# Optimization experiments

Hardware: AMD Instinct MI355X
Metric: run time of the kernel (lower is better)

Reference implementation:

```python
import jax, jax.numpy as jnp
import numpy as np

B, NQ, NK = 2, 1024, 8192
DIM, CTX_DIM = 512, 512
HEADS, DIM_HEAD = 8, 64
INNER = HEADS * DIM_HEAD
EPS = 1e-5
SCALE = DIM_HEAD ** -0.5


def layernorm(x, w, b):
    m = jnp.mean(x, axis=-1, keepdims=True)
    v = jnp.var(x, axis=-1, keepdims=True)
    return (x - m) * jax.lax.rsqrt(v + EPS) * w + b


def rotate_half(x):
    # interleaved pairs: (..., 2i, 2i+1) -> (-x[2i+1], x[2i])
    x1 = x[..., 0::2]
    x2 = x[..., 1::2]
    return jnp.stack((-x2, x1), axis=-1).reshape(x.shape)


def apply_rope(freqs, x):
    # freqs: (b, n, d) broadcast over heads; x: (b, h, n, d)
    f = freqs[:, None, :, :]
    return x * jnp.cos(f) + rotate_half(x) * jnp.sin(f)


def setup_inputs() -> dict:
    key = jax.random.key(0)
    ks = jax.random.split(key, 12)
    x_query = jax.random.normal(ks[0], (B, NQ, DIM), jnp.float32)
    x_context = jax.random.normal(ks[1], (B, NK, CTX_DIM), jnp.float32)
    rotary_q = jax.random.uniform(ks[2], (B, NQ, DIM_HEAD), jnp.float32) * 6.28
    rotary_c = jax.random.uniform(ks[3], (B, NK, DIM_HEAD), jnp.float32) * 6.28
    attn_mask = jax.random.uniform(ks[4], (B, NK)) > 0.1
    attn_mask = attn_mask.at[:, 0].set(True)  # ensure >=1 valid key per row
    s_q = (1.0 / DIM) ** 0.5
    s_c = (1.0 / CTX_DIM) ** 0.5
    s_o = (1.0 / INNER) ** 0.5
    return {
        'x_query': x_query,
        'x_context': x_context,
        'rotary_q': rotary_q,
        'rotary_c': rotary_c,
        'attn_mask': attn_mask,
        'norm_w': jnp.ones((DIM,), jnp.float32),
        'norm_b': jnp.zeros((DIM,), jnp.float32),
        'norm_ctx_w': jnp.ones((CTX_DIM,), jnp.float32),
        'norm_ctx_b': jnp.zeros((CTX_DIM,), jnp.float32),
        'w_q': jax.random.uniform(ks[5], (DIM, INNER), jnp.float32, -s_q, s_q),
        'w_kv': jax.random.uniform(ks[6], (CTX_DIM, 2 * INNER), jnp.float32, -s_c, s_c),
        'w_out': jax.random.uniform(ks[7], (INNER, DIM), jnp.float32, -s_o, s_o),
        'b_out': jax.random.uniform(ks[8], (DIM,), jnp.float32, -s_o, s_o),
    }


def reference(x_query, x_context, rotary_q, rotary_c, attn_mask,
              norm_w, norm_b, norm_ctx_w, norm_ctx_b, w_q, w_kv, w_out, b_out):
    xq = layernorm(x_query, norm_w, norm_b)
    xc = layernorm(x_context, norm_ctx_w, norm_ctx_b)
    q = jnp.einsum('bnd,de->bne', xq, w_q)
    kv = jnp.einsum('bnd,de->bne', xc, w_kv)
    k, v = jnp.split(kv, 2, axis=-1)
    split_heads = lambda t: t.reshape(t.shape[0], t.shape[1], HEADS, DIM_HEAD).transpose(0, 2, 1, 3)
    q, k, v = split_heads(q), split_heads(k), split_heads(v)
    q = apply_rope(rotary_q, q)
    k = apply_rope(rotary_c, k)
    v = apply_rope(rotary_c, v)  # rotate_value=True
    scores = jnp.einsum('bhqd,bhkd->bhqk', q, k) * SCALE
    scores = jnp.where(attn_mask[:, None, None, :], scores, jnp.finfo(scores.dtype).min)
    attn = jax.nn.softmax(scores, axis=-1)
    out = jnp.einsum('bhqk,bhkd->bhqd', attn, v)
    out = apply_rope(-rotary_q, out)  # inverse rotation of output
    out = out.transpose(0, 2, 1, 3).reshape(out.shape[0], NQ, INNER)
    return jnp.einsum('bne,ed->bnd', out, w_out) + b_out
```

## Files before the change

kernel.cpp:

```cpp
#include <hip/hip_runtime.h>
#include <math.h>

typedef __attribute__((ext_vector_type(8))) short  short8;
typedef __attribute__((ext_vector_type(4))) float  f32x4;
typedef __attribute__((ext_vector_type(4))) unsigned short u16x4;
typedef __attribute__((ext_vector_type(8))) unsigned short u16x8;
typedef unsigned short u16;

#define B_     2
#define NQ_    1024
#define NK_    8192
#define DIM_   512
#define H_     8
#define DH_    64
#define EPS_   1e-5f
#define SCALE_ 0.125f
#define LOG2E_ 1.4426950408889634f

__device__ __forceinline__ u16 f2bf(float f) {
  unsigned int u = __float_as_uint(f);
  u += 0x7fffu + ((u >> 16) & 1u);
  return (u16)(u >> 16);
}
__device__ __forceinline__ float fmax3(float a, float b, float c) {
  return fmaxf(fmaxf(a, b), c);
}

__global__ __launch_bounds__(256) void prep_kernel(
    const float* __restrict__ wq, const float* __restrict__ wkv,
    const float* __restrict__ wout,
    const float* __restrict__ xq, const float* __restrict__ xc,
    const float* __restrict__ nw, const float* __restrict__ nb,
    const float* __restrict__ ncw, const float* __restrict__ ncb,
    const float* __restrict__ rq, const float* __restrict__ rc,
    const int* __restrict__ mask,
    u16* __restrict__ wqT, u16* __restrict__ wkvT, u16* __restrict__ woutT,
    u16* __restrict__ xqb, u16* __restrict__ xcb,
    float* __restrict__ cq, float* __restrict__ sq2,
    float* __restrict__ cc, float* __restrict__ sc2,
    float* __restrict__ maskf) {
  __shared__ float tile[64][65];
  const int bid = blockIdx.x;
  const int t = threadIdx.x;
  if (bid < 256) {
    const float* W; u16* WT; int N; int tix;
    if (bid < 64)       { W = wq;   WT = wqT;   N = 512;  tix = bid; }
    else if (bid < 192) { W = wkv;  WT = wkvT;  N = 1024; tix = bid - 64; }
    else                { W = wout; WT = woutT; N = 512;  tix = bid - 192; }
    int ntn = N >> 6;
    int k0 = (tix / ntn) << 6, n0 = (tix % ntn) << 6;
    {
      int kk = t >> 2, nc = (t & 3) << 4;
#pragma unroll
      for (int i = 0; i < 4; ++i) {
        f32x4 v = *(const f32x4*)&W[(size_t)(k0 + kk) * N + n0 + nc + 4 * i];
        tile[kk][nc + 4*i + 0] = v[0];
        tile[kk][nc + 4*i + 1] = v[1];
        tile[kk][nc + 4*i + 2] = v[2];
        tile[kk][nc + 4*i + 3] = v[3];
      }
    }
    __syncthreads();
    {
      int n = t >> 2, kc = (t & 3) << 4;
#pragma unroll
      for (int i = 0; i < 2; ++i) {
        u16x8 o;
#pragma unroll
        for (int j = 0; j < 8; ++j) o[j] = f2bf(tile[kc + 8*i + j][n]);
        *(u16x8*)&WT[(size_t)(n0 + n) * 512 + k0 + kc + 8*i] = o;
      }
    }
  } else if (bid < 4864) {
    int wid = t >> 6, lane = t & 63;
    int row = (bid - 256) * 4 + wid;
    const float* x; const float* w; const float* bb; u16* o; int r;
    if (row < 2048) { x = xq; w = nw;  bb = nb;  o = xqb; r = row; }
    else            { x = xc; w = ncw; bb = ncb; o = xcb; r = row - 2048; }
    const f32x4* px = (const f32x4*)(x + (size_t)r * 512);
    f32x4 v0 = px[lane], v1 = px[lane + 64];
    float s  = v0[0]+v0[1]+v0[2]+v0[3] + v1[0]+v1[1]+v1[2]+v1[3];
    float ss = v0[0]*v0[0]+v0[1]*v0[1]+v0[2]*v0[2]+v0[3]*v0[3]
             + v1[0]*v1[0]+v1[1]*v1[1]+v1[2]*v1[2]+v1[3]*v1[3];
#pragma unroll
    for (int ofs = 32; ofs >= 1; ofs >>= 1) { s += __shfl_xor(s, ofs); ss += __shfl_xor(ss, ofs); }
    float mu = s * (1.f/512.f);
    float var = ss * (1.f/512.f) - mu*mu;
    float rs = rsqrtf(var + EPS_);
    const f32x4* pw = (const f32x4*)w; const f32x4* pb = (const f32x4*)bb;
#pragma unroll
    for (int seg = 0; seg < 2; ++seg) {
      int e4 = lane + 64*seg;
      f32x4 xv = seg ? v1 : v0;
      f32x4 wv = pw[e4], bv = pb[e4];
      u16x4 ov;
#pragma unroll
      for (int c = 0; c < 4; ++c) ov[c] = f2bf((xv[c]-mu)*rs*wv[c] + bv[c]);
      *(u16x4*)&o[(size_t)r*512 + e4*4] = ov;
    }
  } else if (bid < 8960) {
    int i = (bid - 4864) * 256 + t;
    const int NQE = B_*NQ_*DH_;
    const int NCE = B_*NK_*DH_;
    if (i < NQE) { float s, c; sincosf(rq[i], &s, &c); cq[i] = c; sq2[i] = s; }
    if (i < NCE) { float s, c; sincosf(rc[i], &s, &c); cc[i] = c; sc2[i] = s; }
  } else {
    int i = (bid - 8960) * 256 + t;
    maskf[i] = mask[i] ? 1.f : 0.f;
  }
}

template<int MODE>
__global__ __launch_bounds__(256) void gemm_mfma(
    const u16* __restrict__ Abf, const u16* __restrict__ WT,
    const float* __restrict__ ctab, const float* __restrict__ stab,
    const float* __restrict__ bias, const float* __restrict__ mvf,
    u16* __restrict__ out0, u16* __restrict__ out1, float* __restrict__ outf) {
  constexpr int BM   = (MODE==1) ? 128 : 64;
  constexpr int BN   = (MODE==1) ? 128 : 32;
  constexpr int MR   = BM/64;
  constexpr int NR   = BN/16;
  constexpr int N    = (MODE==1) ? 1024 : 512;
  constexpr int NSEQ = (MODE==1) ? 8192 : 1024;
  constexpr int NBN  = N / BN;
  constexpr int NWG  = (((MODE==1)?16384:2048)/BM) * NBN;
  __shared__ u16 As[BM*64];
  __shared__ u16 Bs[BN*64];
  const int tid = threadIdx.x;
  const int w = tid >> 6, l = tid & 63;
  const int la = l >> 4, lb = l & 15;
  int bid = blockIdx.x;
  bid = (bid & 7) * (NWG/8) + (bid >> 3);
  const int m0 = (bid / NBN) * BM;
  const int n0 = (bid % NBN) * BN;
  f32x4 acc[MR][NR];
#pragma unroll
  for (int i = 0; i < MR; ++i)
#pragma unroll
    for (int j = 0; j < NR; ++j) acc[i][j] = (f32x4){0.f,0.f,0.f,0.f};

  constexpr int APT = BM/32;
  constexpr int BPT = BN/32;
  const int arow = tid / (8/APT);
  const int ag0  = (tid % (8/APT)) * APT;
  const int brow = tid / (8/BPT);
  const int bg0  = (tid % (8/BPT)) * BPT;

  auto loadA = [&](int k0, int g) -> short8 {
    if (MODE == 2) {
      int kk = k0 + g*8;
      int m = m0 + arow;
      return *(const short8*)&Abf[((size_t)((m >> 10)*H_ + (kk >> 6)) * NQ_ + (m & 1023)) * 64 + (kk & 63)];
    } else {
      return *(const short8*)&Abf[(size_t)(m0 + arow) * 512 + k0 + g*8];
    }
  };

  short8 apre[APT], bpre[BPT];
#pragma unroll
  for (int i = 0; i < APT; ++i) apre[i] = loadA(0, ag0 + i);
#pragma unroll
  for (int i = 0; i < BPT; ++i) bpre[i] = *(const short8*)&WT[(size_t)(n0 + brow) * 512 + (bg0 + i)*8];

  for (int k0 = 0; k0 < 512; k0 += 64) {
    if (k0) __syncthreads();
#pragma unroll
    for (int i = 0; i < APT; ++i) {
      int g = ag0 + i;
      *(short8*)&As[arow*64 + ((g ^ (arow & 7)) << 3)] = apre[i];
    }
#pragma unroll
    for (int i = 0; i < BPT; ++i) {
      int g = bg0 + i;
      *(short8*)&Bs[brow*64 + ((g ^ (brow & 7)) << 3)] = bpre[i];
    }
    if (k0 + 64 < 512) {
#pragma unroll
      for (int i = 0; i < APT; ++i) apre[i] = loadA(k0 + 64, ag0 + i);
#pragma unroll
      for (int i = 0; i < BPT; ++i) bpre[i] = *(const short8*)&WT[(size_t)(n0 + brow) * 512 + (k0+64) + (bg0 + i)*8];
    }
    __syncthreads();
#pragma unroll
    for (int h = 0; h < 2; ++h) {
      short8 af[MR], bfr[NR];
#pragma unroll
      for (int i = 0; i < MR; ++i) {
        int row = w*(16*MR) + i*16 + lb;
        int g = (4*h + la) ^ (row & 7);
        af[i] = *(const short8*)&As[row*64 + g*8];
      }
#pragma unroll
      for (int j = 0; j < NR; ++j) {
        int row = j*16 + lb;
        int g = (4*h + la) ^ (row & 7);
        bfr[j] = *(const short8*)&Bs[row*64 + g*8];
      }
#pragma unroll
      for (int i = 0; i < MR; ++i)
#pragma unroll
        for (int j = 0; j < NR; ++j)
          acc[i][j] = __builtin_amdgcn_mfma_f32_16x16x32_bf16(af[i], bfr[j], acc[i][j], 0, 0, 0);
    }
  }

  if (MODE == 2) {
#pragma unroll
    for (int i = 0; i < MR; ++i)
#pragma unroll
      for (int j = 0; j < NR; ++j) {
        int n = n0 + 16*j + lb;
        float bv = bias[n];
#pragma unroll
        for (int r = 0; r < 4; ++r) {
          int m = m0 + w*(16*MR) + 16*i + 4*la + r;
          outf[(size_t)m * 512 + n] = acc[i][j][r] + bv;
        }
      }
  } else if (MODE == 1 && n0 >= 512) {
#pragma unroll
    for (int i = 0; i < MR; ++i) {
      int mbase = m0 + w*(16*MR) + 16*i + 4*la;
      int bI = mbase >> 13;
      int seq = mbase & 8191;
      f32x4 mkv = *(const f32x4*)&mvf[mbase];
#pragma unroll
      for (int j = 0; j < NR; ++j) {
        int n = n0 + 16*j + lb;
        int e = n - 512, hh = e >> 6, dh = e & 63;
        u16x4 pk4;
#pragma unroll
        for (int r = 0; r < 4; ++r) {
          int m = mbase + r;
          float x = acc[i][j][r];
          float pr = __shfl_xor(x, 1);
          float cv = ctab[(size_t)m*64 + dh];
          float sv = stab[(size_t)m*64 + dh];
          pk4[r] = f2bf((x*cv + ((n & 1) ? pr*sv : -pr*sv)) * mkv[r]);
        }
        *(u16x4*)&out1[((size_t)(bI*H_ + hh)*64 + dh)*8192 + seq] = pk4;
      }
    }
  } else {
#pragma unroll
    for (int i = 0; i < MR; ++i)
#pragma unroll
      for (int j = 0; j < NR; ++j) {
        int n = n0 + 16*j + lb;
        int hh = n >> 6, dh = n & 63;
#pragma unroll
        for (int r = 0; r < 4; ++r) {
          int m = m0 + w*(16*MR) + 16*i + 4*la + r;
          float x = acc[i][j][r];
          float pr = __shfl_xor(x, 1);
          float cv = ctab[(size_t)m*64 + dh];
          float sv = stab[(size_t)m*64 + dh];
          float y = x*cv + ((n & 1) ? pr*sv : -pr*sv);
          if (MODE == 0) y *= SCALE_ * LOG2E_;
          int bI = m / NSEQ, seq = m % NSEQ;
          out0[((size_t)(bI*H_ + hh) * NSEQ + seq) * 64 + dh] = f2bf(y);
        }
      }
  }
}

template<int NS>
__global__ __launch_bounds__(512) void attn_mfma(
    const u16* __restrict__ qb, const u16* __restrict__ kb,
    const u16* __restrict__ vtg, const float* __restrict__ maskf,
    float* __restrict__ Opart, float* __restrict__ mpart, float* __restrict__ lpart) {
  __shared__ u16 Ks[64*64];
  __shared__ u16 Vt[64*64];
  __shared__ u16 Ps[8*16*64];
  constexpr int NWG = 16*8*NS;
  constexpr int CH  = NWG/8;
  constexpr int LS  = (NS==8) ? 3 : 2;
  int orig = blockIdx.x;
  int wid = (orig & 7) * CH + (orig >> 3);
  const int qt = wid & 7;
  const int s  = (wid >> 3) & (NS-1);
  const int bh = wid >> (3 + LS);
  const int bI = bh >> 3;
  const int tid = threadIdx.x;
  const int w = tid >> 6, l = tid & 63;
  const int la = l >> 4, lb = l & 15;
  const int key0 = s * (NK_/NS);

  const int qrow = qt*128 + w*16 + lb;
  short8 qf0 = *(const short8*)&qb[(((size_t)bh * NQ_) + qrow) * 64 + 8*la];
  short8 qf1 = *(const short8*)&qb[(((size_t)bh * NQ_) + qrow) * 64 + 32 + 8*la];

  const int krow = tid >> 3;
  const int kg   = tid & 7;
  const u16* kptr = kb  + ((size_t)bh * NK_ + key0 + krow) * 64;
  const u16* vptr = vtg + ((size_t)bh * 64 + krow) * 8192 + key0;
  short8 kpre = *(const short8*)&kptr[kg*8];
  short8 vpre = *(const short8*)&vptr[kg*8];
  const int ksw = krow & 7;
  const float* mrow = maskf + bI*8192 + key0 + 4*la;

  f32x4 accO[4];
#pragma unroll
  for (int j = 0; j < 4; ++j) accO[j] = (f32x4){0.f,0.f,0.f,0.f};
  float m_run = -1e30f, l_run = 0.f;
  constexpr int NT = (NK_/NS)/64;

  const int pbase = (w*16 + lb)*64;
  const int pwofs = (4*la) & 7;

  for (int kt = 0; kt < NT; ++kt) {
    *(short8*)&Ks[krow*64 + ((kg ^ ksw) << 3)] = kpre;
    *(short8*)&Vt[krow*64 + ((kg ^ ksw) << 3)] = vpre;
    if (kt + 1 < NT) {
      kpre = *(const short8*)&kptr[(kt+1)*4096 + kg*8];
      vpre = *(const short8*)&vptr[(kt+1)*64 + kg*8];
    }
    __syncthreads();

    f32x4 sc[4];
#pragma unroll
    for (int t = 0; t < 4; ++t) sc[t] = (f32x4){0.f,0.f,0.f,0.f};
    __builtin_amdgcn_s_setprio(1);
#pragma unroll
    for (int t = 0; t < 4; ++t) {
      int row = t*16 + lb;
      int g0 = la ^ (row & 7);
      int g1 = (4 + la) ^ (row & 7);
      short8 kf0 = *(const short8*)&Ks[row*64 + g0*8];
      short8 kf1 = *(const short8*)&Ks[row*64 + g1*8];
      sc[t] = __builtin_amdgcn_mfma_f32_16x16x32_bf16(kf0, qf0, sc[t], 0, 0, 0);
      sc[t] = __builtin_amdgcn_mfma_f32_16x16x32_bf16(kf1, qf1, sc[t], 0, 0, 0);
    }
    __builtin_amdgcn_s_setprio(0);
    float a0 = fmax3(sc[0][0], sc[0][1], sc[0][2]);
    float a1 = fmax3(sc[0][3], sc[1][0], sc[1][1]);
    float a2 = fmax3(sc[1][2], sc[1][3], sc[2][0]);
    float a3 = fmax3(sc[2][1], sc[2][2], sc[2][3]);
    float a4 = fmax3(sc[3][0], sc[3][1], sc[3][2]);
    float pmax = fmaxf(fmax3(a0, a1, a2), fmax3(a3, a4, sc[3][3]));
    pmax = fmaxf(pmax, __shfl_xor(pmax, 16));
    pmax = fmaxf(pmax, __shfl_xor(pmax, 32));
    if (!__all(pmax <= m_run + 11.f)) {
      float mnew = fmaxf(m_run, pmax);
      float scl = __builtin_amdgcn_exp2f(m_run - mnew);
      m_run = mnew;
      l_run *= scl;
      float sr[4];
#pragma unroll
      for (int r = 0; r < 4; ++r) sr[r] = __shfl(scl, (l & 48) | (4*la + r));
#pragma unroll
      for (int j = 0; j < 4; ++j)
#pragma unroll
        for (int r = 0; r < 4; ++r) accO[j][r] *= sr[r];
    }
    float l_add = 0.f;
#pragma unroll
    for (int t = 0; t < 4; ++t) {
      f32x4 mk = *(const f32x4*)&mrow[kt*64 + t*16];
      float p0 = __builtin_amdgcn_exp2f(sc[t][0] - m_run);
      float p1 = __builtin_amdgcn_exp2f(sc[t][1] - m_run);
      float p2 = __builtin_amdgcn_exp2f(sc[t][2] - m_run);
      float p3 = __builtin_amdgcn_exp2f(sc[t][3] - m_run);
      l_add = fmaf(p0, mk[0], l_add);
      l_add = fmaf(p1, mk[1], l_add);
      l_add = fmaf(p2, mk[2], l_add);
      l_add = fmaf(p3, mk[3], l_add);
      int gst = 2*t + (la >> 1);
      uint2 pp;
      asm("v_cvt_pk_bf16_f32 %0, %1, %2" : "=v"(pp.x) : "v"(p0), "v"(p1));
      asm("v_cvt_pk_bf16_f32 %0, %1, %2" : "=v"(pp.y) : "v"(p2), "v"(p3));
      *(uint2*)&Ps[pbase + ((gst ^ (lb & 7)) << 3) + pwofs] = pp;
    }
    l_run += l_add;
    __builtin_amdgcn_s_setprio(1);
#pragma unroll
    for (int kh = 0; kh < 2; ++kh) {
      int pg = (4*kh + la) ^ (lb & 7);
      short8 pf = *(const short8*)&Ps[pbase + pg*8];
#pragma unroll
      for (int j = 0; j < 4; ++j) {
        int d = j*16 + lb;
        int vg = (4*kh + la) ^ (d & 7);
        short8 vf = *(const short8*)&Vt[d*64 + vg*8];
        accO[j] = __builtin_amdgcn_mfma_f32_16x16x32_bf16(pf, vf, accO[j], 0, 0, 0);
      }
    }
    __builtin_amdgcn_s_setprio(0);
    __syncthreads();
  }

  l_run += __shfl_xor(l_run, 16);
  l_run += __shfl_xor(l_run, 32);

  const int qa = qt*128 + w*16;
  const size_t obase = ((size_t)s*16 + bh) * 1024;
#pragma unroll
  for (int j = 0; j < 4; ++j)
#pragma unroll
    for (int r = 0; r < 4; ++r)
      Opart[(obase + qa + 4*la + r) * 64 + j*16 + lb] = accO[j][r];
  if (la == 0) {
    mpart[obase + qa + lb] = m_run;
    lpart[obase + qa + lb] = l_run;
  }
}

template<int NS>
__global__ __launch_bounds__(256) void combine_kernel(
    const float* __restrict__ Opart, const float* __restrict__ mpart,
    const float* __restrict__ lpart,
    const float* __restrict__ cosq, const float* __restrict__ sinq,
    u16* __restrict__ aob) {
  const int bid = blockIdx.x;
  const int bh = bid >> 4, qt = bid & 15;
  const int t = threadIdx.x;
  const int ql = t >> 2, ds = (t & 3) << 4;
  const int q = qt*64 + ql;
  const int bI = bh >> 3;
  const size_t rbase = ((size_t)bh << 10) + q;
  float m[NS], li[NS];
  float M = -1e30f;
#pragma unroll
  for (int s = 0; s < NS; ++s) {
    m[s]  = mpart[(size_t)s*16384 + rbase];
    li[s] = lpart[(size_t)s*16384 + rbase];
    M = fmaxf(M, m[s]);
  }
  float ws[NS]; float den = 0.f;
#pragma unroll
  for (int s = 0; s < NS; ++s) { ws[s] = __builtin_amdgcn_exp2f(m[s] - M); den += ws[s]*li[s]; }
  float inv = 1.f / den;
  u16 ob[16];
#pragma unroll
  for (int c = 0; c < 4; ++c) {
    int d0 = ds + 4*c;
    f32x4 o = (f32x4){0.f,0.f,0.f,0.f};
#pragma unroll
    for (int s = 0; s < NS; ++s) {
      f32x4 v = *(const f32x4*)&Opart[((size_t)s*16384 + rbase)*64 + d0];
      o += ws[s] * v;
    }
    o *= inv;
    size_t tix = ((((size_t)bI << 10) + q) << 6) + d0;
    f32x4 cv = *(const f32x4*)&cosq[tix];
    f32x4 sv = *(const f32x4*)&sinq[tix];
    ob[4*c+0] = f2bf(o[0]*cv[0] + o[1]*sv[0]);
    ob[4*c+1] = f2bf(o[1]*cv[1] - o[0]*sv[1]);
    ob[4*c+2] = f2bf(o[2]*cv[2] + o[3]*sv[2]);
    ob[4*c+3] = f2bf(o[3]*cv[3] - o[2]*sv[3]);
  }
  u16x8 w0, w1;
#pragma unroll
  for (int j = 0; j < 8; ++j) { w0[j] = ob[j]; w1[j] = ob[8+j]; }
  *(u16x8*)&aob[rbase*64 + ds]     = w0;
  *(u16x8*)&aob[rbase*64 + ds + 8] = w1;
}

extern "C" void kernel_launch(void* const* d_in, const int* in_sizes, int n_in,
                              void* d_out, int out_size, void* d_ws, size_t ws_size,
                              hipStream_t stream) {
  (void)in_sizes; (void)n_in; (void)out_size;
  const float* xq   = (const float*)d_in[0];
  const float* xc   = (const float*)d_in[1];
  const float* rq   = (const float*)d_in[2];
  const float* rc   = (const float*)d_in[3];
  const int*   mask = (const int*)d_in[4];
  const float* nw   = (const float*)d_in[5];
  const float* nb   = (const float*)d_in[6];
  const float* ncw  = (const float*)d_in[7];
  const float* ncb  = (const float*)d_in[8];
  const float* wq   = (const float*)d_in[9];
  const float* wkv  = (const float*)d_in[10];
  const float* wout = (const float*)d_in[11];
  const float* bout = (const float*)d_in[12];
  float* out = (float*)d_out;

  char* p = (char*)d_ws;
  u16*   woutT  = (u16*)p;   p += 524288;
  float* cosq   = (float*)p; p += 524288;
  float* sinq   = (float*)p; p += 524288;
  u16*   qb     = (u16*)p;   p += 2097152;
  u16*   kb     = (u16*)p;   p += 16777216;
  u16*   vtg    = (u16*)p;   p += 16777216;
  float* mpart4 = (float*)p; p += 262144;
  float* lpart4 = (float*)p; p += 262144;
  u16*   aob    = (u16*)p;   p += 2097152;
  float* maskf  = (float*)aob;
  char* pool = p;
  u16*   wqT   = (u16*)p;   p += 524288;
  u16*   wkvT  = (u16*)p;   p += 1048576;
  u16*   xqb   = (u16*)p;   p += 2097152;
  u16*   xcb   = (u16*)p;   p += 16777216;
  float* cosc  = (float*)p; p += 4194304;
  float* sinc  = (float*)p; p += 4194304;
  float* Opart = (float*)pool;
  float* mpart8 = (float*)(pool + 33554432);
  float* lpart8 = (float*)(pool + 33554432 + 524288);
  const size_t need8 = (size_t)(pool - (char*)d_ws) + 33554432ull + 1048576ull;
  const bool use8 = ws_size >= need8;

  prep_kernel<<<dim3(9024), dim3(256), 0, stream>>>(
      wq, wkv, wout, xq, xc, nw, nb, ncw, ncb, rq, rc, mask,
      wqT, wkvT, woutT, xqb, xcb, cosq, sinq, cosc, sinc, maskf);
  gemm_mfma<0><<<dim3(512), dim3(256), 0, stream>>>(
      xqb, wqT, cosq, sinq, nullptr, nullptr, qb, nullptr, nullptr);
  gemm_mfma<1><<<dim3(1024), dim3(256), 0, stream>>>(
      xcb, wkvT, cosc, sinc, nullptr, maskf, kb, vtg, nullptr);
  if (use8) {
    attn_mfma<8><<<dim3(1024), dim3(512), 0, stream>>>(
        qb, kb, vtg, maskf, Opart, mpart8, lpart8);
    combine_kernel<8><<<dim3(256), dim3(256), 0, stream>>>(
        Opart, mpart8, lpart8, cosq, sinq, aob);
  } else {
    attn_mfma<4><<<dim3(512), dim3(512), 0, stream>>>(
        qb, kb, vtg, maskf, Opart, mpart4, lpart4);
    combine_kernel<4><<<dim3(256), dim3(256), 0, stream>>>(
        Opart, mpart4, lpart4, cosq, sinq, aob);
  }
  gemm_mfma<2><<<dim3(512), dim3(256), 0, stream>>>(
      aob, woutT, nullptr, nullptr, bout, nullptr, nullptr, nullptr, out);
}
```

Before: 209.2 us.

## Merge Q and KV projection launches and retile attention to 64 queries × 128 keys

The Q and KV projection GEMMs now share a single launch, with a device-function body and shared memory passed in, which removes one kernel launch and lets the two run concurrently. The attention kernel moves from 512-thread blocks over 128 queries and 64-key tiles to 256-thread blocks over 64 queries and 128-key tiles, processed as two 64-key chunks per barrier. Split-K is fixed at 4 splits, so the 8-split path that depended on workspace size is gone. This halves the number of barriers and global-load rounds per key, at the cost of fewer waves per block and more shared memory per block.

```diff
diff --git a/kernel.cpp b/kernel.cpp
--- a/kernel.cpp
+++ b/kernel.cpp
@@ -111,7 +111,8 @@
 }
 
 template<int MODE>
-__global__ __launch_bounds__(256) void gemm_mfma(
+__device__ __forceinline__ void gemm_body(
+    int bid0, u16* __restrict__ smem,
     const u16* __restrict__ Abf, const u16* __restrict__ WT,
     const float* __restrict__ ctab, const float* __restrict__ stab,
     const float* __restrict__ bias, const float* __restrict__ mvf,
@@ -124,13 +125,12 @@
   constexpr int NSEQ = (MODE==1) ? 8192 : 1024;
   constexpr int NBN  = N / BN;
   constexpr int NWG  = (((MODE==1)?16384:2048)/BM) * NBN;
-  __shared__ u16 As[BM*64];
-  __shared__ u16 Bs[BN*64];
+  u16* As = smem;
+  u16* Bs = smem + BM*64;
   const int tid = threadIdx.x;
   const int w = tid >> 6, l = tid & 63;
   const int la = l >> 4, lb = l & 15;
-  int bid = blockIdx.x;
-  bid = (bid & 7) * (NWG/8) + (bid >> 3);
+  int bid = (bid0 & 7) * (NWG/8) + (bid0 >> 3);
   const int m0 = (bid / NBN) * BM;
   const int n0 = (bid % NBN) * BN;
   f32x4 acc[MR][NR];
@@ -264,135 +264,178 @@
   }
 }
 
+__global__ __launch_bounds__(256) void qkv_kernel(
+    const u16* __restrict__ xqb, const u16* __restrict__ wqT,
+    const u16* __restrict__ xcb, const u16* __restrict__ wkvT,
+    const float* __restrict__ cosq, const float* __restrict__ sinq,
+    const float* __restrict__ cosc, const float* __restrict__ sinc,
+    const float* __restrict__ maskf,
+    u16* __restrict__ qb, u16* __restrict__ kb, u16* __restrict__ vtg) {
+  __shared__ u16 smem[16384];
+  int b = blockIdx.x;
+  if (b < 512) {
+    gemm_body<0>(b, smem, xqb, wqT, cosq, sinq, nullptr, nullptr, qb, nullptr, nullptr);
+  } else {
+    gemm_body<1>(b - 512, smem, xcb, wkvT, cosc, sinc, nullptr, maskf, kb, vtg, nullptr);
+  }
+}
+
+__global__ __launch_bounds__(256) void gemm2_kernel(
+    const u16* __restrict__ aob, const u16* __restrict__ woutT,
+    const float* __restrict__ bias, float* __restrict__ out) {
+  __shared__ u16 smem[6144];
+  gemm_body<2>(blockIdx.x, smem, aob, woutT, nullptr, nullptr, bias, nullptr,
+               nullptr, nullptr, out);
+}
+
 template<int NS>
-__global__ __launch_bounds__(512) void attn_mfma(
+__global__ __launch_bounds__(256) void attn_mfma(
     const u16* __restrict__ qb, const u16* __restrict__ kb,
     const u16* __restrict__ vtg, const float* __restrict__ maskf,
     float* __restrict__ Opart, float* __restrict__ mpart, float* __restrict__ lpart) {
-  __shared__ u16 Ks[64*64];
-  __shared__ u16 Vt[64*64];
-  __shared__ u16 Ps[8*16*64];
-  constexpr int NWG = 16*8*NS;
+  __shared__ u16 Ks[128*64];
+  __shared__ u16 Vt[64*128];
+  __shared__ u16 Ps[4*16*64];
+  constexpr int NWG = 16*16*NS;
   constexpr int CH  = NWG/8;
   constexpr int LS  = (NS==8) ? 3 : 2;
   int orig = blockIdx.x;
   int wid = (orig & 7) * CH + (orig >> 3);
-  const int qt = wid & 7;
-  const int s  = (wid >> 3) & (NS-1);
-  const int bh = wid >> (3 + LS);
+  const int qt = wid & 15;
+  const int s  = (wid >> 4) & (NS-1);
+  const int bh = wid >> (4 + LS);
   const int bI = bh >> 3;
   const int tid = threadIdx.x;
   const int w = tid >> 6, l = tid & 63;
   const int la = l >> 4, lb = l & 15;
   const int key0 = s * (NK_/NS);
 
-  const int qrow = qt*128 + w*16 + lb;
+  const int qrow = qt*64 + w*16 + lb;
   short8 qf0 = *(const short8*)&qb[(((size_t)bh * NQ_) + qrow) * 64 + 8*la];
   short8 qf1 = *(const short8*)&qb[(((size_t)bh * NQ_) + qrow) * 64 + 32 + 8*la];
 
-  const int krow = tid >> 3;
-  const int kg   = tid & 7;
+  const int krow = tid >> 1;
+  const int kg0  = (tid & 1) * 4;
+  const int vd   = tid >> 2;
+  const int vg0  = (tid & 3) * 4;
   const u16* kptr = kb  + ((size_t)bh * NK_ + key0 + krow) * 64;
-  const u16* vptr = vtg + ((size_t)bh * 64 + krow) * 8192 + key0;
-  short8 kpre = *(const short8*)&kptr[kg*8];
-  short8 vpre = *(const short8*)&vptr[kg*8];
-  const int ksw = krow & 7;
+  const u16* vptr = vtg + ((size_t)bh * 64 + vd) * 8192 + key0;
+  const int ksw = krow & 7, vsw = vd & 7;
+  short8 kpre0 = *(const short8*)&kptr[(kg0+0)*8];
+  short8 kpre1 = *(const short8*)&kptr[(kg0+1)*8];
+  short8 vpre0 = *(const short8*)&vptr[(vg0+0)*8];
+  short8 vpre1 = *(const short8*)&vptr[(vg0+1)*8];
   const float* mrow = maskf + bI*8192 + key0 + 4*la;
 
   f32x4 accO[4];
 #pragma unroll
   for (int j = 0; j < 4; ++j) accO[j] = (f32x4){0.f,0.f,0.f,0.f};
   float m_run = -1e30f, l_run = 0.f;
-  constexpr int NT = (NK_/NS)/64;
+  constexpr int NT = (NK_/NS)/128;
 
   const int pbase = (w*16 + lb)*64;
   const int pwofs = (4*la) & 7;
 
   for (int kt = 0; kt < NT; ++kt) {
-    *(short8*)&Ks[krow*64 + ((kg ^ ksw) << 3)] = kpre;
-    *(short8*)&Vt[krow*64 + ((kg ^ ksw) << 3)] = vpre;
+    short8 k2 = *(const short8*)&kptr[(size_t)kt*8192 + (kg0+2)*8];
+    short8 k3 = *(const short8*)&kptr[(size_t)kt*8192 + (kg0+3)*8];
+    short8 v2 = *(const short8*)&vptr[kt*128 + (vg0+2)*8];
+    short8 v3 = *(const short8*)&vptr[kt*128 + (vg0+3)*8];
+    *(short8*)&Ks[krow*64 + (((kg0+0) ^ ksw) << 3)] = kpre0;
+    *(short8*)&Ks[krow*64 + (((kg0+1) ^ ksw) << 3)] = kpre1;
+    *(short8*)&Vt[vd*128 + (((vg0+0) ^ vsw) << 3)] = vpre0;
+    *(short8*)&Vt[vd*128 + (((vg0+1) ^ vsw) << 3)] = vpre1;
+    *(short8*)&Ks[krow*64 + (((kg0+2) ^ ksw) << 3)] = k2;
+    *(short8*)&Ks[krow*64 + (((kg0+3) ^ ksw) << 3)] = k3;
+    *(short8*)&Vt[vd*128 + (((vg0+2) ^ vsw) << 3)] = v2;
+    *(short8*)&Vt[vd*128 + (((vg0+3) ^ vsw) << 3)] = v3;
     if (kt + 1 < NT) {
-      kpre = *(const short8*)&kptr[(kt+1)*4096 + kg*8];
-      vpre = *(const short8*)&vptr[(kt+1)*64 + kg*8];
+      kpre0 = *(const short8*)&kptr[(size_t)(kt+1)*8192 + (kg0+0)*8];
+      kpre1 = *(const short8*)&kptr[(size_t)(kt+1)*8192 + (kg0+1)*8];
+      vpre0 = *(const short8*)&vptr[(kt+1)*128 + (vg0+0)*8];
+      vpre1 = *(const short8*)&vptr[(kt+1)*128 + (vg0+1)*8];
     }
     __syncthreads();
 
-    f32x4 sc[4];
-#pragma unroll
-    for (int t = 0; t < 4; ++t) sc[t] = (f32x4){0.f,0.f,0.f,0.f};
-    __builtin_amdgcn_s_setprio(1);
-#pragma unroll
-    for (int t = 0; t < 4; ++t) {
-      int row = t*16 + lb;
-      int g0 = la ^ (row & 7);
-      int g1 = (4 + la) ^ (row & 7);
-      short8 kf0 = *(const short8*)&Ks[row*64 + g0*8];
-      short8 kf1 = *(const short8*)&Ks[row*64 + g1*8];
-      sc[t] = __builtin_amdgcn_mfma_f32_16x16x32_bf16(kf0, qf0, sc[t], 0, 0, 0);
-      sc[t] = __builtin_amdgcn_mfma_f32_16x16x32_bf16(kf1, qf1, sc[t], 0, 0, 0);
-    }
-    __builtin_amdgcn_s_setprio(0);
-    float a0 = fmax3(sc[0][0], sc[0][1], sc[0][2]);
-    float a1 = fmax3(sc[0][3], sc[1][0], sc[1][1]);
-    float a2 = fmax3(sc[1][2], sc[1][3], sc[2][0]);
-    float a3 = fmax3(sc[2][1], sc[2][2], sc[2][3]);
-    float a4 = fmax3(sc[3][0], sc[3][1], sc[3][2]);
-    float pmax = fmaxf(fmax3(a0, a1, a2), fmax3(a3, a4, sc[3][3]));
-    pmax = fmaxf(pmax, __shfl_xor(pmax, 16));
-    pmax = fmaxf(pmax, __shfl_xor(pmax, 32));
-    if (!__all(pmax <= m_run + 11.f)) {
-      float mnew = fmaxf(m_run, pmax);
-      float scl = __builtin_amdgcn_exp2f(m_run - mnew);
-      m_run = mnew;
-      l_run *= scl;
-      float sr[4];
-#pragma unroll
-      for (int r = 0; r < 4; ++r) sr[r] = __shfl(scl, (l & 48) | (4*la + r));
-#pragma unroll
-      for (int j = 0; j < 4; ++j)
-#pragma unroll
-        for (int r = 0; r < 4; ++r) accO[j][r] *= sr[r];
-    }
-    float l_add = 0.f;
-#pragma unroll
-    for (int t = 0; t < 4; ++t) {
-      f32x4 mk = *(const f32x4*)&mrow[kt*64 + t*16];
-      float p0 = __builtin_amdgcn_exp2f(sc[t][0] - m_run);
-      float p1 = __builtin_amdgcn_exp2f(sc[t][1] - m_run);
-      float p2 = __builtin_amdgcn_exp2f(sc[t][2] - m_run);
-      float p3 = __builtin_amdgcn_exp2f(sc[t][3] - m_run);
-      l_add = fmaf(p0, mk[0], l_add);
-      l_add = fmaf(p1, mk[1], l_add);
-      l_add = fmaf(p2, mk[2], l_add);
-      l_add = fmaf(p3, mk[3], l_add);
-      int gst = 2*t + (la >> 1);
-      uint2 pp;
-      asm("v_cvt_pk_bf16_f32 %0, %1, %2" : "=v"(pp.x) : "v"(p0), "v"(p1));
-      asm("v_cvt_pk_bf16_f32 %0, %1, %2" : "=v"(pp.y) : "v"(p2), "v"(p3));
-      *(uint2*)&Ps[pbase + ((gst ^ (lb & 7)) << 3) + pwofs] = pp;
-    }
-    l_run += l_add;
-    __builtin_amdgcn_s_setprio(1);
-#pragma unroll
-    for (int kh = 0; kh < 2; ++kh) {
-      int pg = (4*kh + la) ^ (lb & 7);
-      short8 pf = *(const short8*)&Ps[pbase + pg*8];
-#pragma unroll
-      for (int j = 0; j < 4; ++j) {
-        int d = j*16 + lb;
-        int vg = (4*kh + la) ^ (d & 7);
-        short8 vf = *(const short8*)&Vt[d*64 + vg*8];
-        accO[j] = __builtin_amdgcn_mfma_f32_16x16x32_bf16(pf, vf, accO[j], 0, 0, 0);
-      }
-    }
-    __builtin_amdgcn_s_setprio(0);
+#pragma unroll
+    for (int c = 0; c < 2; ++c) {
+      f32x4 sc[4];
+#pragma unroll
+      for (int t = 0; t < 4; ++t) sc[t] = (f32x4){0.f,0.f,0.f,0.f};
+      __builtin_amdgcn_s_setprio(1);
+#pragma unroll
+      for (int t = 0; t < 4; ++t) {
+        int row = c*64 + t*16 + lb;
+        int g0 = la ^ (row & 7);
+        int g1 = (4 + la) ^ (row & 7);
+        short8 kf0 = *(const short8*)&Ks[row*64 + g0*8];
+        short8 kf1 = *(const short8*)&Ks[row*64 + g1*8];
+        sc[t] = __builtin_amdgcn_mfma_f32_16x16x32_bf16(kf0, qf0, sc[t], 0, 0, 0);
+        sc[t] = __builtin_amdgcn_mfma_f32_16x16x32_bf16(kf1, qf1, sc[t], 0, 0, 0);
+      }
+      __builtin_amdgcn_s_setprio(0);
+      float a0 = fmax3(sc[0][0], sc[0][1], sc[0][2]);
+      float a1 = fmax3(sc[0][3], sc[1][0], sc[1][1]);
+      float a2 = fmax3(sc[1][2], sc[1][3], sc[2][0]);
+      float a3 = fmax3(sc[2][1], sc[2][2], sc[2][3]);
+      float a4 = fmax3(sc[3][0], sc[3][1], sc[3][2]);
+      float pmax = fmaxf(fmax3(a0, a1, a2), fmax3(a3, a4, sc[3][3]));
+      pmax = fmaxf(pmax, __shfl_xor(pmax, 16));
+      pmax = fmaxf(pmax, __shfl_xor(pmax, 32));
+      if (!__all(pmax <= m_run + 11.f)) {
+        float mnew = fmaxf(m_run, pmax);
+        float scl = __builtin_amdgcn_exp2f(m_run - mnew);
+        m_run = mnew;
+        l_run *= scl;
+        float sr[4];
+#pragma unroll
+        for (int r = 0; r < 4; ++r) sr[r] = __shfl(scl, (l & 48) | (4*la + r));
+#pragma unroll
+        for (int j = 0; j < 4; ++j)
+#pragma unroll
+          for (int r = 0; r < 4; ++r) accO[j][r] *= sr[r];
+      }
+      float l_add = 0.f;
+#pragma unroll
+      for (int t = 0; t < 4; ++t) {
+        f32x4 mk = *(const f32x4*)&mrow[kt*128 + c*64 + t*16];
+        float p0 = __builtin_amdgcn_exp2f(sc[t][0] - m_run);
+        float p1 = __builtin_amdgcn_exp2f(sc[t][1] - m_run);
+        float p2 = __builtin_amdgcn_exp2f(sc[t][2] - m_run);
+        float p3 = __builtin_amdgcn_exp2f(sc[t][3] - m_run);
+        l_add = fmaf(p0, mk[0], l_add);
+        l_add = fmaf(p1, mk[1], l_add);
+        l_add = fmaf(p2, mk[2], l_add);
+        l_add = fmaf(p3, mk[3], l_add);
+        int gst = 2*t + (la >> 1);
+        uint2 pp;
+        asm("v_cvt_pk_bf16_f32 %0, %1, %2" : "=v"(pp.x) : "v"(p0), "v"(p1));
+        asm("v_cvt_pk_bf16_f32 %0, %1, %2" : "=v"(pp.y) : "v"(p2), "v"(p3));
+        *(uint2*)&Ps[pbase + ((gst ^ (lb & 7)) << 3) + pwofs] = pp;
+      }
+      l_run += l_add;
+      __builtin_amdgcn_s_setprio(1);
+#pragma unroll
+      for (int kh = 0; kh < 2; ++kh) {
+        int pg = (4*kh + la) ^ (lb & 7);
+        short8 pf = *(const short8*)&Ps[pbase + pg*8];
+#pragma unroll
+        for (int j = 0; j < 4; ++j) {
+          int d = j*16 + lb;
+          int vg = (c*8 + 4*kh + la) ^ (d & 7);
+          short8 vf = *(const short8*)&Vt[d*128 + vg*8];
+          accO[j] = __builtin_amdgcn_mfma_f32_16x16x32_bf16(pf, vf, accO[j], 0, 0, 0);
+        }
+      }
+      __builtin_amdgcn_s_setprio(0);
+    }
     __syncthreads();
   }
 
   l_run += __shfl_xor(l_run, 16);
   l_run += __shfl_xor(l_run, 32);
 
-  const int qa = qt*128 + w*16;
+  const int qa = qt*64 + w*16;
   const size_t obase = ((size_t)s*16 + bh) * 1024;
 #pragma unroll
   for (int j = 0; j < 4; ++j)
@@ -459,7 +502,7 @@
 extern "C" void kernel_launch(void* const* d_in, const int* in_sizes, int n_in,
                               void* d_out, int out_size, void* d_ws, size_t ws_size,
                               hipStream_t stream) {
-  (void)in_sizes; (void)n_in; (void)out_size;
+  (void)in_sizes; (void)n_in; (void)out_size; (void)ws_size;
   const float* xq   = (const float*)d_in[0];
   const float* xc   = (const float*)d_in[1];
   const float* rq   = (const float*)d_in[2];
@@ -494,29 +537,15 @@
   float* cosc  = (float*)p; p += 4194304;
   float* sinc  = (float*)p; p += 4194304;
   float* Opart = (float*)pool;
-  float* mpart8 = (float*)(pool + 33554432);
-  float* lpart8 = (float*)(pool + 33554432 + 524288);
-  const size_t need8 = (size_t)(pool - (char*)d_ws) + 33554432ull + 1048576ull;
-  const bool use8 = ws_size >= need8;
 
   prep_kernel<<<dim3(9024), dim3(256), 0, stream>>>(
       wq, wkv, wout, xq, xc, nw, nb, ncw, ncb, rq, rc, mask,
       wqT, wkvT, woutT, xqb, xcb, cosq, sinq, cosc, sinc, maskf);
-  gemm_mfma<0><<<dim3(512), dim3(256), 0, stream>>>(
-      xqb, wqT, cosq, sinq, nullptr, nullptr, qb, nullptr, nullptr);
-  gemm_mfma<1><<<dim3(1024), dim3(256), 0, stream>>>(
-      xcb, wkvT, cosc, sinc, nullptr, maskf, kb, vtg, nullptr);
-  if (use8) {
-    attn_mfma<8><<<dim3(1024), dim3(512), 0, stream>>>(
-        qb, kb, vtg, maskf, Opart, mpart8, lpart8);
-    combine_kernel<8><<<dim3(256), dim3(256), 0, stream>>>(
-        Opart, mpart8, lpart8, cosq, sinq, aob);
-  } else {
-    attn_mfma<4><<<dim3(512), dim3(512), 0, stream>>>(
-        qb, kb, vtg, maskf, Opart, mpart4, lpart4);
-    combine_kernel<4><<<dim3(256), dim3(256), 0, stream>>>(
-        Opart, mpart4, lpart4, cosq, sinq, aob);
-  }
-  gemm_mfma<2><<<dim3(512), dim3(256), 0, stream>>>(
-      aob, woutT, nullptr, nullptr, bout, nullptr, nullptr, nullptr, out);
-}
+  qkv_kernel<<<dim3(1536), dim3(256), 0, stream>>>(
+      xqb, wqT, xcb, wkvT, cosq, sinq, cosc, sinc, maskf, qb, kb, vtg);
+  attn_mfma<4><<<dim3(1024), dim3(256), 0, stream>>>(
+      qb, kb, vtg, maskf, Opart, mpart4, lpart4);
+  combine_kernel<4><<<dim3(256), dim3(256), 0, stream>>>(
+      Opart, mpart4, lpart4, cosq, sinq, aob);
+  gemm2_kernel<<<dim3(512), dim3(256), 0, stream>>>(aob, woutT, bout, out);
+}
```

After: 223.2 us. 6.7% more time.
